# Kernel tuning notes

Hardware: AMD Instinct MI355X
Metric: run time of the kernel (lower is better)

Reference implementation:

```python
import jax, jax.numpy as jnp
import numpy as np

DIM = 128
H = W = 56
NUM_HEADS = 4
WS = 7            # window size
SHIFT = 3
N = WS * WS       # tokens per window (49)
EPS = 1e-5


def _relative_position_index():
    coords = np.stack(np.meshgrid(np.arange(WS), np.arange(WS), indexing='ij'))  # [2,ws,ws]
    cf = coords.reshape(2, -1)                                                   # [2,N]
    rel = cf[:, :, None] - cf[:, None, :]                                        # [2,N,N]
    rel = rel.transpose(1, 2, 0).astype(np.int64)                                # [N,N,2]
    rel[:, :, 0] += WS - 1
    rel[:, :, 1] += WS - 1
    rel[:, :, 0] *= 2 * WS - 1
    return rel.sum(-1)  # [N,N]


def _attn_mask():
    # shifted-window attention mask, [nW, N, N] with 0 / -100
    img = np.zeros((H, W), dtype=np.float32)
    cnt = 0
    for hs in (slice(0, -WS), slice(-WS, -SHIFT), slice(-SHIFT, None)):
        for ws_ in (slice(0, -WS), slice(-WS, -SHIFT), slice(-SHIFT, None)):
            img[hs, ws_] = cnt
            cnt += 1
    mw = img.reshape(H // WS, WS, W // WS, WS).transpose(0, 2, 1, 3).reshape(-1, N)  # [nW,N]
    diff = mw[:, None, :] - mw[:, :, None]
    return np.where(diff != 0, -100.0, 0.0).astype(np.float32)


_RPI = jnp.asarray(_relative_position_index())
_MASK = jnp.asarray(_attn_mask())


def _layernorm(x, g, b):
    mu = jnp.mean(x, axis=-1, keepdims=True)
    var = jnp.mean(jnp.square(x - mu), axis=-1, keepdims=True)
    return (x - mu) * jax.lax.rsqrt(var + EPS) * g + b


def _window_partition(x):
    # x: [B,H,W,C] -> [B*nW, N, C]
    B, _, _, C = x.shape
    x = x.reshape(B, H // WS, WS, W // WS, WS, C).transpose(0, 1, 3, 2, 4, 5)
    return x.reshape(-1, N, C)


def _window_reverse(w, B):
    # [B*nW, N, C] -> [B,H,W,C]
    C = w.shape[-1]
    x = w.reshape(B, H // WS, W // WS, WS, WS, C).transpose(0, 1, 3, 2, 4, 5)
    return x.reshape(B, H, W, C)


def setup_inputs() -> dict:
    key = jax.random.key(0)
    ks = jax.random.split(key, 8)
    B, L, C = 64, H * W, DIM
    hid = 4 * DIM
    s = 0.02
    return {
        'x': jax.random.normal(ks[0], (B, L, C), jnp.float32),
        'norm1_g': jnp.ones((C,), jnp.float32),
        'norm1_b': jnp.zeros((C,), jnp.float32),
        'qkv_w': jax.random.normal(ks[1], (C, 3 * C), jnp.float32) * s,
        'qkv_b': jnp.zeros((3 * C,), jnp.float32),
        'rel_bias_table': jax.random.normal(ks[2], ((2 * WS - 1) ** 2, NUM_HEADS), jnp.float32) * s,
        'proj_w': jax.random.normal(ks[3], (C, C), jnp.float32) * s,
        'proj_b': jnp.zeros((C,), jnp.float32),
        'norm2_g': jnp.ones((C,), jnp.float32),
        'norm2_b': jnp.zeros((C,), jnp.float32),
        'fc1_w': jax.random.normal(ks[4], (C, hid), jnp.float32) * s,
        'fc1_b': jnp.zeros((hid,), jnp.float32),
        'fc2_w': jax.random.normal(ks[5], (hid, C), jnp.float32) * s,
        'fc2_b': jnp.zeros((C,), jnp.float32),
    }


def reference(x, norm1_g, norm1_b, qkv_w, qkv_b, rel_bias_table, proj_w, proj_b,
              norm2_g, norm2_b, fc1_w, fc1_b, fc2_w, fc2_b):
    B, L, C = x.shape
    hdim = C // NUM_HEADS
    scale = hdim ** -0.5

    shortcut = x
    xn = _layernorm(x, norm1_g, norm1_b).reshape(B, H, W, C)

    # cyclic shift (H,W divisible by WS -> no padding)
    xs = jnp.roll(xn, shift=(-SHIFT, -SHIFT), axis=(1, 2))
    xw = _window_partition(xs)                      # [B*nW, N, C]
    B_ = xw.shape[0]
    nW = B_ // B

    # window attention
    qkv = xw @ qkv_w + qkv_b                        # [B_,N,3C]
    qkv = qkv.reshape(B_, N, 3, NUM_HEADS, hdim).transpose(2, 0, 3, 1, 4)
    q, k, v = qkv[0], qkv[1], qkv[2]                # [B_,h,N,d]
    attn = jnp.einsum('bhnd,bhmd->bhnm', q * scale, k)
    bias = rel_bias_table[_RPI.reshape(-1)].reshape(N, N, NUM_HEADS)
    attn = attn + bias.transpose(2, 0, 1)[None]
    attn = attn.reshape(B, nW, NUM_HEADS, N, N) + _MASK[None, :, None]
    attn = jax.nn.softmax(attn.reshape(B_, NUM_HEADS, N, N), axis=-1)
    out = jnp.einsum('bhnm,bhmd->bhnd', attn, v)
    out = out.transpose(0, 2, 1, 3).reshape(B_, N, C)
    out = out @ proj_w + proj_b

    # reverse windows, un-shift
    xr = _window_reverse(out, B)
    xr = jnp.roll(xr, shift=(SHIFT, SHIFT), axis=(1, 2))
    x = shortcut + xr.reshape(B, L, C)

    # MLP with exact GELU (torch nn.GELU default)
    xn2 = _layernorm(x, norm2_g, norm2_b)
    h = jax.nn.gelu(xn2 @ fc1_w + fc1_b, approximate=False)
    x = x + (h @ fc2_w + fc2_b)
    return x
```

## Files before the change

### kernel.cpp

```cpp
#include <hip/hip_runtime.h>
#include <cstdint>

#define DIM   128
#define NH    4
#define WSZ   7
#define NTOK  49
#define SHIFT 3
#define HIMG  56
#define BATCH 64
#define LTOK  3136
#define HID   512
#define EPSF  1e-5f

typedef short bf16x8 __attribute__((ext_vector_type(8)));
typedef float f32x4  __attribute__((ext_vector_type(4)));

__device__ __forceinline__ float bf2f(ushort u){ return __uint_as_float(((uint32_t)u)<<16); }
__device__ __forceinline__ ushort f2bf(float f){
  uint32_t u = __float_as_uint(f);
  u += 0x7FFFu + ((u>>16)&1u);
  return (ushort)(u>>16);
}
__device__ __forceinline__ float wred(float v){
  #pragma unroll
  for (int off=32; off; off>>=1) v += __shfl_xor(v, off, 64);
  return v;
}

__global__ __launch_bounds__(256) void transpose_cvt_all(
    const float* __restrict__ qkvw, const float* __restrict__ pw,
    const float* __restrict__ f1w,  const float* __restrict__ f2w,
    ushort* __restrict__ ws)
{
  int bid = blockIdx.x;
  const float* src; ushort* dst; int R, Cc, b0;
  if (bid < 192)      { src = qkvw; dst = ws;          R = 128; Cc = 384; b0 = 0;   }
  else if (bid < 256) { src = pw;   dst = ws + 49152;  R = 128; Cc = 128; b0 = 192; }
  else if (bid < 512) { src = f1w;  dst = ws + 65536;  R = 128; Cc = 512; b0 = 256; }
  else                { src = f2w;  dst = ws + 131072; R = 512; Cc = 128; b0 = 512; }
  int idx = (bid - b0)*256 + threadIdx.x;
  int c = idx / R, r = idx % R;
  dst[idx] = f2bf(src[r*Cc + c]);
}

#define OFF_BUFA 0
#define OFF_QK   8704
#define QKSTR    40
#define OFF_TBL  (OFF_QK + 8*NTOK*QKSTR)
#define OFF_PP   (OFF_QK + 12936)
#define SMEM_SZ  25072

__global__ __launch_bounds__(256,3) void swin_block_kernel(
    const float* __restrict__ x, const float* __restrict__ n1g, const float* __restrict__ n1b,
    const ushort* __restrict__ qkv_wt, const float* __restrict__ qkvb,
    const float* __restrict__ bias_tbl, const ushort* __restrict__ proj_wt,
    const float* __restrict__ projb,
    const float* __restrict__ n2g, const float* __restrict__ n2b,
    const ushort* __restrict__ fc1_wt, const float* __restrict__ fc1b,
    const ushort* __restrict__ fc2_wt, const float* __restrict__ fc2b,
    float* __restrict__ out)
{
  __shared__ ushort smem[SMEM_SZ];

  const int tid  = threadIdx.x;
  const int wave = tid >> 6;
  const int lane = tid & 63;
  const int b_   = blockIdx.x;
  const int b    = b_ >> 6;
  const int win  = b_ & 63;
  const int wi   = win >> 3, wj = win & 7;

  const int ncol  = lane & 15;
  const int quad  = lane >> 4;
  const int koff  = quad * 8;
  const int rbase = quad * 4;
  const int l32   = lane & 31;
  const int hlf   = lane >> 5;

  for (int i = tid; i < 676; i += 256) smem[OFF_TBL + i] = f2bf(bias_tbl[i]);

  {
    const int c = lane*2;
    const float g0 = n1g[c], g1 = n1g[c+1], be0 = n1b[c], be1 = n1b[c+1];
    for (int r = wave; r < NTOK; r += 4){
      int ti = r / 7, tj = r % 7;
      int hh = (wi*7 + ti + SHIFT) % HIMG;
      int ww = (wj*7 + tj + SHIFT) % HIMG;
      size_t base = ((size_t)b * LTOK + hh*HIMG + ww) * DIM;
      float2 tv = *(const float2*)(x + base + c);
      float v0 = tv.x, v1 = tv.y;
      float mu = wred(v0 + v1) * (1.0f/128.0f);
      float d0 = v0-mu, d1 = v1-mu;
      float rstd = rsqrtf(wred(d0*d0 + d1*d1)*(1.0f/128.0f) + EPSF);
      smem[OFF_BUFA + r*136 + c]   = f2bf(d0*rstd*g0 + be0);
      smem[OFF_BUFA + r*136 + c+1] = f2bf(d1*rstd*g1 + be1);
    }
  }
  __syncthreads();

  {
    bf16x8 afrag[4][4];
    #pragma unroll
    for (int mt=0; mt<4; mt++)
      #pragma unroll
      for (int kb=0; kb<4; kb++)
        afrag[mt][kb] = *(const bf16x8*)&smem[OFF_BUFA + (mt*16 + ncol)*136 + kb*32 + koff];
    __syncthreads();

    for (int i = tid; i < 128*15; i += 256){
      int dd = i/15, t = 49 + i%15;
      smem[OFF_BUFA + dd*68 + t] = 0;
    }

    #pragma unroll
    for (int nt=0; nt<6; nt++){
      int c = wave*96 + nt*16 + ncol;
      int which = c >> 7, head = (c >> 5) & 3, d = c & 31;
      bf16x8 bfrag[4];
      #pragma unroll
      for (int kb=0; kb<4; kb++) bfrag[kb] = *(const bf16x8*)(qkv_wt + (size_t)c*128 + kb*32 + koff);
      float bias = qkvb[c];
      int qkb = OFF_QK + (head*2 + which)*NTOK*QKSTR + d;
      int vb  = OFF_BUFA + (head*32 + d)*68;
      #pragma unroll
      for (int mt=0; mt<4; mt++){
        f32x4 acc = {0.f,0.f,0.f,0.f};
        #pragma unroll
        for (int kb=0; kb<4; kb++)
          acc = __builtin_amdgcn_mfma_f32_16x16x32_bf16(afrag[mt][kb], bfrag[kb], acc, 0,0,0);
        #pragma unroll
        for (int r=0; r<4; r++){
          int m = mt*16 + rbase + r;
          if (m < NTOK){
            ushort v = f2bf(acc[r] + bias);
            if (which == 2) smem[vb + m] = v;
            else            smem[qkb + m*QKSTR] = v;
          }
        }
      }
    }
  }
  __syncthreads();

  {
    const int h = wave;
    const int qbase = OFF_QK + (h*2    )*NTOK*QKSTR;
    const int kbase = OFF_QK + (h*2 + 1)*NTOK*QKSTR;
    const int pbase = qbase;

    bf16x8 qf[4], kf[4];
    #pragma unroll
    for (int mt=0; mt<4; mt++) qf[mt] = *(const bf16x8*)&smem[qbase + (mt*16 + ncol)*QKSTR + koff];
    #pragma unroll
    for (int nt=0; nt<4; nt++) kf[nt] = *(const bf16x8*)&smem[kbase + (nt*16 + ncol)*QKSTR + koff];

    f32x4 s[4][4];
    #pragma unroll
    for (int mt=0; mt<4; mt++)
      #pragma unroll
      for (int nt=0; nt<4; nt++){
        f32x4 z = {0.f,0.f,0.f,0.f};
        s[mt][nt] = __builtin_amdgcn_mfma_f32_16x16x32_bf16(qf[mt], kf[nt], z, 0,0,0);
      }

    int kcol[4], rm[4];
    #pragma unroll
    for (int nt=0; nt<4; nt++){
      int k = nt*16 + ncol;
      kcol[nt] = k;
      int kc = k < NTOK ? k : 48;
      int si = kc/7, sj = kc%7;
      int sh = wi*7 + si, sw = wj*7 + sj;
      rm[nt] = (sh<49?0:(sh<53?1:2))*3 + (sw<49?0:(sw<53?1:2));
    }
    const float scale = 0.17677669529663687f;

    #pragma unroll
    for (int mt=0; mt<4; mt++){
      #pragma unroll
      for (int r=0; r<4; r++){
        int m  = mt*16 + rbase + r;
        int mc = m < NTOK ? m : 48;
        int ti = mc/7, tj = mc%7;
        int habs = wi*7 + ti, wabs = wj*7 + tj;
        int rn = (habs<49?0:(habs<53?1:2))*3 + (wabs<49?0:(wabs<53?1:2));
        float sv[4];
        #pragma unroll
        for (int nt=0; nt<4; nt++){
          int k  = kcol[nt];
          int kc = k < NTOK ? k : 48;
          int si = kc/7, sj = kc%7;
          int idx = (ti - si + 6)*13 + (tj - sj + 6);
          float bias = bf2f(smem[OFF_TBL + idx*4 + h]);
          float v = s[mt][nt][r]*scale + bias + (rn == rm[nt] ? 0.f : -100.f);
          sv[nt] = (k < NTOK) ? v : -1e30f;
        }
        float sum = 0.f;
        #pragma unroll
        for (int nt=0; nt<4; nt++){ sv[nt] = __expf(sv[nt]); sum += sv[nt]; }
        #pragma unroll
        for (int off=1; off<16; off<<=1) sum += __shfl_xor(sum, off, 64);
        float rs = 1.0f/sum;
        #pragma unroll
        for (int nt=0; nt<4; nt++) s[mt][nt][r] = sv[nt]*rs;
      }
    }

    #pragma unroll
    for (int mt=0; mt<4; mt++)
      #pragma unroll
      for (int r=0; r<4; r++){
        int m = mt*16 + rbase + r;
        if (m < NTOK){
          #pragma unroll
          for (int nt=0; nt<4; nt++)
            smem[pbase + m*72 + kcol[nt]] = f2bf(s[mt][nt][r]);
        }
      }

    bf16x8 vf[2][2];
    #pragma unroll
    for (int nt=0; nt<2; nt++)
      #pragma unroll
      for (int kq=0; kq<2; kq++)
        vf[nt][kq] = *(const bf16x8*)&smem[OFF_BUFA + (h*32 + nt*16 + ncol)*68 + kq*32 + koff];
    __syncthreads();

    f32x4 o[4][2];
    #pragma unroll
    for (int mt=0; mt<4; mt++)
      #pragma unroll
      for (int nt=0; nt<2; nt++){ f32x4 z={0.f,0.f,0.f,0.f}; o[mt][nt]=z; }

    #pragma unroll
    for (int mt=0; mt<4; mt++)
      #pragma unroll
      for (int kq=0; kq<2; kq++){
        bf16x8 pf = *(const bf16x8*)&smem[pbase + (mt*16 + ncol)*72 + kq*32 + koff];
        #pragma unroll
        for (int nt=0; nt<2; nt++)
          o[mt][nt] = __builtin_amdgcn_mfma_f32_16x16x32_bf16(pf, vf[nt][kq], o[mt][nt], 0,0,0);
      }

    #pragma unroll
    for (int mt=0; mt<4; mt++)
      #pragma unroll
      for (int nt=0; nt<2; nt++)
        #pragma unroll
        for (int r=0; r<4; r++){
          int m = mt*16 + rbase + r;
          if (m < NTOK)
            smem[OFF_BUFA + m*136 + h*32 + nt*16 + ncol] = f2bf(o[mt][nt][r]);
        }
  }
  __syncthreads();

  float* xstage = (float*)&smem[OFF_QK];
  {
    for (int rr = wave*2 + hlf; rr < NTOK; rr += 8){
      int ti = rr/7, tj = rr%7;
      int hh = (wi*7 + ti + SHIFT) % HIMG;
      int ww = (wj*7 + tj + SHIFT) % HIMG;
      float4 v = *(const float4*)(x + ((size_t)b*LTOK + hh*HIMG + ww)*DIM + l32*4);
      *(float4*)&xstage[rr*132 + l32*4] = v;
    }
  }

  float x2reg[2][4][4];
  {
    bf16x8 afrag[4][4];
    #pragma unroll
    for (int mt=0; mt<4; mt++)
      #pragma unroll
      for (int kb=0; kb<4; kb++)
        afrag[mt][kb] = *(const bf16x8*)&smem[OFF_BUFA + (mt*16 + ncol)*136 + kb*32 + koff];
    __syncthreads();

    #pragma unroll
    for (int nt=0; nt<2; nt++){
      int j = wave*32 + nt*16 + ncol;
      bf16x8 bfrag[4];
      #pragma unroll
      for (int kb=0; kb<4; kb++) bfrag[kb] = *(const bf16x8*)(proj_wt + (size_t)j*128 + kb*32 + koff);
      float bias = projb[j];
      #pragma unroll
      for (int mt=0; mt<4; mt++){
        f32x4 acc = {0.f,0.f,0.f,0.f};
        #pragma unroll
        for (int kb=0; kb<4; kb++)
          acc = __builtin_amdgcn_mfma_f32_16x16x32_bf16(afrag[mt][kb], bfrag[kb], acc, 0,0,0);
        #pragma unroll
        for (int r=0; r<4; r++){
          int m = mt*16 + rbase + r;
          if (m < NTOK) x2reg[nt][mt][r] = acc[r] + bias + xstage[m*132 + j];
          else          x2reg[nt][mt][r] = 0.f;
        }
      }
    }
  }

  float2* pp = (float2*)&smem[OFF_PP];
  #pragma unroll
  for (int mt=0; mt<4; mt++)
    #pragma unroll
    for (int r=0; r<4; r++){
      float a0 = x2reg[0][mt][r], a1 = x2reg[1][mt][r];
      float sm = a0 + a1, sq = a0*a0 + a1*a1;
      #pragma unroll
      for (int off=1; off<16; off<<=1){ sm += __shfl_xor(sm, off, 64); sq += __shfl_xor(sq, off, 64); }
      if (ncol == 0) pp[(mt*16 + rbase + r)*4 + wave] = make_float2(sm, sq);
    }
  __syncthreads();

  {
    const int j0 = wave*32 + ncol, j1 = j0 + 16;
    const float g0 = n2g[j0], be0 = n2b[j0], g1 = n2g[j1], be1 = n2b[j1];
    #pragma unroll
    for (int mt=0; mt<4; mt++)
      #pragma unroll
      for (int r=0; r<4; r++){
        int m = mt*16 + rbase + r;
        f32x4 pa = *(const f32x4*)&pp[m*4];
        f32x4 pb = *(const f32x4*)&pp[m*4 + 2];
        float sm = pa[0]+pa[2]+pb[0]+pb[2];
        float sq = pa[1]+pa[3]+pb[1]+pb[3];
        float mu   = sm * (1.0f/128.0f);
        float rstd = rsqrtf(sq*(1.0f/128.0f) - mu*mu + EPSF);
        smem[OFF_BUFA + m*136 + j0] = f2bf((x2reg[0][mt][r]-mu)*rstd*g0 + be0);
        smem[OFF_BUFA + m*136 + j1] = f2bf((x2reg[1][mt][r]-mu)*rstd*g1 + be1);
      }
  }
  __syncthreads();

  f32x4 o2[2][4];
  #pragma unroll
  for (int nt=0; nt<2; nt++)
    #pragma unroll
    for (int mt=0; mt<4; mt++){ f32x4 z={0.f,0.f,0.f,0.f}; o2[nt][mt]=z; }

  for (int hk=0; hk<4; hk++){
    #pragma unroll
    for (int nt=0; nt<2; nt++){
      int cloc = wave*32 + nt*16 + ncol;
      int c = hk*128 + cloc;
      bf16x8 bfrag[4];
      #pragma unroll
      for (int kb=0; kb<4; kb++)
        bfrag[kb] = *(const bf16x8*)(fc1_wt + (size_t)c*128 + kb*32 + koff);
      float bias = fc1b[c];
      #pragma unroll
      for (int mt=0; mt<4; mt++){
        f32x4 acc = {0.f,0.f,0.f,0.f};
        #pragma unroll
        for (int kb=0; kb<4; kb++){
          bf16x8 a = *(const bf16x8*)&smem[OFF_BUFA + (mt*16 + ncol)*136 + kb*32 + koff];
          acc = __builtin_amdgcn_mfma_f32_16x16x32_bf16(a, bfrag[kb], acc, 0,0,0);
        }
        #pragma unroll
        for (int r=0; r<4; r++){
          int m = mt*16 + rbase + r;
          if (mt < 3 || m < NTOK){
            float v = acc[r] + bias;
            float g = 0.5f*v*(1.0f + erff(v*0.70710678118654752f));
            smem[OFF_QK + m*136 + cloc] = f2bf(g);
          }
        }
      }
    }
    __syncthreads();

    #pragma unroll
    for (int nt=0; nt<2; nt++){
      int j = wave*32 + nt*16 + ncol;
      bf16x8 bfrag[4];
      #pragma unroll
      for (int kb=0; kb<4; kb++)
        bfrag[kb] = *(const bf16x8*)(fc2_wt + (size_t)j*512 + hk*128 + kb*32 + koff);
      #pragma unroll
      for (int mt=0; mt<4; mt++){
        #pragma unroll
        for (int kb=0; kb<4; kb++){
          bf16x8 a = *(const bf16x8*)&smem[OFF_QK + (mt*16 + ncol)*136 + kb*32 + koff];
          o2[nt][mt] = __builtin_amdgcn_mfma_f32_16x16x32_bf16(a, bfrag[kb], o2[nt][mt], 0,0,0);
        }
      }
    }
    __syncthreads();
  }

  float* fout = (float*)&smem[OFF_QK];
  #pragma unroll
  for (int nt=0; nt<2; nt++){
    int j = wave*32 + nt*16 + ncol;
    float bias = fc2b[j];
    #pragma unroll
    for (int mt=0; mt<4; mt++){
      #pragma unroll
      for (int r=0; r<4; r++){
        int m = mt*16 + rbase + r;
        if (m < NTOK)
          fout[m*132 + j] = o2[nt][mt][r] + bias + x2reg[nt][mt][r];
      }
    }
  }
  __syncthreads();

  for (int rr = wave*2 + hlf; rr < NTOK; rr += 8){
    int ti = rr/7, tj = rr%7;
    int hh = (wi*7 + ti + SHIFT) % HIMG;
    int ww = (wj*7 + tj + SHIFT) % HIMG;
    float4 v = *(const float4*)&fout[rr*132 + l32*4];
    *(float4*)(out + ((size_t)b*LTOK + hh*HIMG + ww)*DIM + l32*4) = v;
  }
}

extern "C" void kernel_launch(void* const* d_in, const int* in_sizes, int n_in,
                              void* d_out, int out_size, void* d_ws, size_t ws_size,
                              hipStream_t stream)
{
  const float* x    = (const float*)d_in[0];
  const float* n1g  = (const float*)d_in[1];
  const float* n1b  = (const float*)d_in[2];
  const float* qkvw = (const float*)d_in[3];
  const float* qkvb = (const float*)d_in[4];
  const float* tbl  = (const float*)d_in[5];
  const float* pw   = (const float*)d_in[6];
  const float* pb   = (const float*)d_in[7];
  const float* n2g  = (const float*)d_in[8];
  const float* n2b  = (const float*)d_in[9];
  const float* f1w  = (const float*)d_in[10];
  const float* f1b  = (const float*)d_in[11];
  const float* f2w  = (const float*)d_in[12];
  const float* f2b  = (const float*)d_in[13];

  ushort* wsbase = (ushort*)d_ws;
  transpose_cvt_all<<<768, 256, 0, stream>>>(qkvw, pw, f1w, f2w, wsbase);

  swin_block_kernel<<<4096, 256, 0, stream>>>(x, n1g, n1b, wsbase, qkvb, tbl,
                                              wsbase + 49152, pb, n2g, n2b,
                                              wsbase + 65536, f1b, wsbase + 131072, f2b,
                                              (float*)d_out);
}
```

Baseline: 531.3 us.

## Tile weight transpose, vectorize LN1, prefetch residual, reuse MLP A-fragments, fast GELU

Several changes land together. The weight transpose kernel now goes through a padded shared-memory tile so both reads and writes are coalesced. LayerNorm1 now uses float4 loads with half-wave reductions. The residual x rows are prefetched into registers before the attention PV stage instead of being loaded after it. The MLP loops load each A fragment from LDS once and use it for both column tiles. Exact erff is replaced by an Abramowitz-Stegun polynomial erf using rcp and exp, which adds some approximation error (about 1e-7 absolute), and the prefetch registers may raise register pressure.

```diff
diff --git a/kernel.cpp b/kernel.cpp
--- a/kernel.cpp
+++ b/kernel.cpp
@@ -21,10 +21,15 @@
   u += 0x7FFFu + ((u>>16)&1u);
   return (ushort)(u>>16);
 }
-__device__ __forceinline__ float wred(float v){
-  #pragma unroll
-  for (int off=32; off; off>>=1) v += __shfl_xor(v, off, 64);
-  return v;
+
+__device__ __forceinline__ float gelu_f(float v){
+  float xa = fabsf(v) * 0.70710678118654752f;
+  float t  = __builtin_amdgcn_rcpf(fmaf(0.3275911f, xa, 1.0f));
+  float p  = fmaf(fmaf(fmaf(fmaf(1.061405429f, t, -1.453152027f), t,
+                       1.421413741f), t, -0.284496736f), t, 0.254829592f) * t;
+  float e  = __expf(-xa*xa);
+  float er = copysignf(fmaf(-p, e, 1.0f), v);
+  return 0.5f * v * (1.0f + er);
 }
 
 __global__ __launch_bounds__(256) void transpose_cvt_all(
@@ -32,15 +37,28 @@
     const float* __restrict__ f1w,  const float* __restrict__ f2w,
     ushort* __restrict__ ws)
 {
+  __shared__ ushort tile[32][33];
   int bid = blockIdx.x;
   const float* src; ushort* dst; int R, Cc, b0;
-  if (bid < 192)      { src = qkvw; dst = ws;          R = 128; Cc = 384; b0 = 0;   }
-  else if (bid < 256) { src = pw;   dst = ws + 49152;  R = 128; Cc = 128; b0 = 192; }
-  else if (bid < 512) { src = f1w;  dst = ws + 65536;  R = 128; Cc = 512; b0 = 256; }
-  else                { src = f2w;  dst = ws + 131072; R = 512; Cc = 128; b0 = 512; }
-  int idx = (bid - b0)*256 + threadIdx.x;
-  int c = idx / R, r = idx % R;
-  dst[idx] = f2bf(src[r*Cc + c]);
+  if (bid < 48)       { src = qkvw; dst = ws;          R = 128; Cc = 384; b0 = 0;   }
+  else if (bid < 64)  { src = pw;   dst = ws + 49152;  R = 128; Cc = 128; b0 = 48;  }
+  else if (bid < 128) { src = f1w;  dst = ws + 65536;  R = 128; Cc = 512; b0 = 64;  }
+  else                { src = f2w;  dst = ws + 131072; R = 512; Cc = 128; b0 = 128; }
+  int t = bid - b0;
+  int tpr = Cc >> 5;
+  int tr = t / tpr, tc = t % tpr;
+  int tx = threadIdx.x & 31, ty = threadIdx.x >> 5;
+  #pragma unroll
+  for (int k = 0; k < 4; k++){
+    int r = tr*32 + ty + k*8;
+    tile[ty + k*8][tx] = f2bf(src[(size_t)r*Cc + tc*32 + tx]);
+  }
+  __syncthreads();
+  #pragma unroll
+  for (int k = 0; k < 4; k++){
+    int c = tc*32 + ty + k*8;
+    dst[(size_t)c*R + tr*32 + tx] = tile[tx][ty + k*8];
+  }
 }
 
 #define OFF_BUFA 0
@@ -80,20 +98,29 @@
   for (int i = tid; i < 676; i += 256) smem[OFF_TBL + i] = f2bf(bias_tbl[i]);
 
   {
-    const int c = lane*2;
-    const float g0 = n1g[c], g1 = n1g[c+1], be0 = n1b[c], be1 = n1b[c+1];
-    for (int r = wave; r < NTOK; r += 4){
+    const int c = l32*4;
+    const float4 g4 = *(const float4*)(n1g + c);
+    const float4 b4 = *(const float4*)(n1b + c);
+    for (int r = wave*2 + hlf; r < NTOK; r += 8){
       int ti = r / 7, tj = r % 7;
       int hh = (wi*7 + ti + SHIFT) % HIMG;
       int ww = (wj*7 + tj + SHIFT) % HIMG;
-      size_t base = ((size_t)b * LTOK + hh*HIMG + ww) * DIM;
-      float2 tv = *(const float2*)(x + base + c);
-      float v0 = tv.x, v1 = tv.y;
-      float mu = wred(v0 + v1) * (1.0f/128.0f);
-      float d0 = v0-mu, d1 = v1-mu;
-      float rstd = rsqrtf(wred(d0*d0 + d1*d1)*(1.0f/128.0f) + EPSF);
-      smem[OFF_BUFA + r*136 + c]   = f2bf(d0*rstd*g0 + be0);
-      smem[OFF_BUFA + r*136 + c+1] = f2bf(d1*rstd*g1 + be1);
+      float4 tv = *(const float4*)(x + ((size_t)b*LTOK + hh*HIMG + ww)*DIM + c);
+      float sm = tv.x + tv.y + tv.z + tv.w;
+      #pragma unroll
+      for (int off=16; off; off>>=1) sm += __shfl_xor(sm, off, 64);
+      float mu = sm * (1.0f/128.0f);
+      float d0 = tv.x-mu, d1 = tv.y-mu, d2 = tv.z-mu, d3 = tv.w-mu;
+      float sq = d0*d0 + d1*d1 + d2*d2 + d3*d3;
+      #pragma unroll
+      for (int off=16; off; off>>=1) sq += __shfl_xor(sq, off, 64);
+      float rstd = rsqrtf(sq*(1.0f/128.0f) + EPSF);
+      ushort4 o;
+      o.x = f2bf(d0*rstd*g4.x + b4.x);
+      o.y = f2bf(d1*rstd*g4.y + b4.y);
+      o.z = f2bf(d2*rstd*g4.z + b4.z);
+      o.w = f2bf(d3*rstd*g4.w + b4.w);
+      *(ushort4*)&smem[OFF_BUFA + r*136 + c] = o;
     }
   }
   __syncthreads();
@@ -141,6 +168,8 @@
     }
   }
   __syncthreads();
+
+  float4 xpre[7];
 
   {
     const int h = wave;
@@ -207,6 +236,17 @@
     }
 
     #pragma unroll
+    for (int kk=0; kk<7; kk++){
+      int rr = wave*2 + hlf + kk*8;
+      if (rr < NTOK){
+        int ti = rr/7, tj = rr%7;
+        int hh = (wi*7 + ti + SHIFT) % HIMG;
+        int ww = (wj*7 + tj + SHIFT) % HIMG;
+        xpre[kk] = *(const float4*)(x + ((size_t)b*LTOK + hh*HIMG + ww)*DIM + l32*4);
+      }
+    }
+
+    #pragma unroll
     for (int mt=0; mt<4; mt++)
       #pragma unroll
       for (int r=0; r<4; r++){
@@ -256,14 +296,10 @@
   __syncthreads();
 
   float* xstage = (float*)&smem[OFF_QK];
-  {
-    for (int rr = wave*2 + hlf; rr < NTOK; rr += 8){
-      int ti = rr/7, tj = rr%7;
-      int hh = (wi*7 + ti + SHIFT) % HIMG;
-      int ww = (wj*7 + tj + SHIFT) % HIMG;
-      float4 v = *(const float4*)(x + ((size_t)b*LTOK + hh*HIMG + ww)*DIM + l32*4);
-      *(float4*)&xstage[rr*132 + l32*4] = v;
-    }
+  #pragma unroll
+  for (int kk=0; kk<7; kk++){
+    int rr = wave*2 + hlf + kk*8;
+    if (rr < NTOK) *(float4*)&xstage[rr*132 + l32*4] = xpre[kk];
   }
 
   float x2reg[2][4][4];
@@ -339,50 +375,61 @@
     for (int mt=0; mt<4; mt++){ f32x4 z={0.f,0.f,0.f,0.f}; o2[nt][mt]=z; }
 
   for (int hk=0; hk<4; hk++){
-    #pragma unroll
-    for (int nt=0; nt<2; nt++){
-      int cloc = wave*32 + nt*16 + ncol;
-      int c = hk*128 + cloc;
-      bf16x8 bfrag[4];
-      #pragma unroll
-      for (int kb=0; kb<4; kb++)
-        bfrag[kb] = *(const bf16x8*)(fc1_wt + (size_t)c*128 + kb*32 + koff);
-      float bias = fc1b[c];
+    {
+      bf16x8 bfrag2[2][4];
+      float  bias2[2];
+      #pragma unroll
+      for (int nt=0; nt<2; nt++){
+        int c = hk*128 + wave*32 + nt*16 + ncol;
+        #pragma unroll
+        for (int kb=0; kb<4; kb++)
+          bfrag2[nt][kb] = *(const bf16x8*)(fc1_wt + (size_t)c*128 + kb*32 + koff);
+        bias2[nt] = fc1b[c];
+      }
       #pragma unroll
       for (int mt=0; mt<4; mt++){
-        f32x4 acc = {0.f,0.f,0.f,0.f};
-        #pragma unroll
-        for (int kb=0; kb<4; kb++){
-          bf16x8 a = *(const bf16x8*)&smem[OFF_BUFA + (mt*16 + ncol)*136 + kb*32 + koff];
-          acc = __builtin_amdgcn_mfma_f32_16x16x32_bf16(a, bfrag[kb], acc, 0,0,0);
-        }
-        #pragma unroll
-        for (int r=0; r<4; r++){
-          int m = mt*16 + rbase + r;
-          if (mt < 3 || m < NTOK){
-            float v = acc[r] + bias;
-            float g = 0.5f*v*(1.0f + erff(v*0.70710678118654752f));
-            smem[OFF_QK + m*136 + cloc] = f2bf(g);
+        bf16x8 a4[4];
+        #pragma unroll
+        for (int kb=0; kb<4; kb++)
+          a4[kb] = *(const bf16x8*)&smem[OFF_BUFA + (mt*16 + ncol)*136 + kb*32 + koff];
+        #pragma unroll
+        for (int nt=0; nt<2; nt++){
+          f32x4 acc = {0.f,0.f,0.f,0.f};
+          #pragma unroll
+          for (int kb=0; kb<4; kb++)
+            acc = __builtin_amdgcn_mfma_f32_16x16x32_bf16(a4[kb], bfrag2[nt][kb], acc, 0,0,0);
+          int cloc = wave*32 + nt*16 + ncol;
+          #pragma unroll
+          for (int r=0; r<4; r++){
+            int m = mt*16 + rbase + r;
+            if (mt < 3 || m < NTOK)
+              smem[OFF_QK + m*136 + cloc] = f2bf(gelu_f(acc[r] + bias2[nt]));
           }
         }
       }
     }
     __syncthreads();
 
-    #pragma unroll
-    for (int nt=0; nt<2; nt++){
-      int j = wave*32 + nt*16 + ncol;
-      bf16x8 bfrag[4];
-      #pragma unroll
-      for (int kb=0; kb<4; kb++)
-        bfrag[kb] = *(const bf16x8*)(fc2_wt + (size_t)j*512 + hk*128 + kb*32 + koff);
+    {
+      bf16x8 bfrag2[2][4];
+      #pragma unroll
+      for (int nt=0; nt<2; nt++){
+        int j = wave*32 + nt*16 + ncol;
+        #pragma unroll
+        for (int kb=0; kb<4; kb++)
+          bfrag2[nt][kb] = *(const bf16x8*)(fc2_wt + (size_t)j*512 + hk*128 + kb*32 + koff);
+      }
       #pragma unroll
       for (int mt=0; mt<4; mt++){
-        #pragma unroll
-        for (int kb=0; kb<4; kb++){
-          bf16x8 a = *(const bf16x8*)&smem[OFF_QK + (mt*16 + ncol)*136 + kb*32 + koff];
-          o2[nt][mt] = __builtin_amdgcn_mfma_f32_16x16x32_bf16(a, bfrag[kb], o2[nt][mt], 0,0,0);
-        }
+        bf16x8 ha4[4];
+        #pragma unroll
+        for (int kb=0; kb<4; kb++)
+          ha4[kb] = *(const bf16x8*)&smem[OFF_QK + (mt*16 + ncol)*136 + kb*32 + koff];
+        #pragma unroll
+        for (int nt=0; nt<2; nt++)
+          #pragma unroll
+          for (int kb=0; kb<4; kb++)
+            o2[nt][mt] = __builtin_amdgcn_mfma_f32_16x16x32_bf16(ha4[kb], bfrag2[nt][kb], o2[nt][mt], 0,0,0);
       }
     }
     __syncthreads();
@@ -434,7 +481,7 @@
   const float* f2b  = (const float*)d_in[13];
 
   ushort* wsbase = (ushort*)d_ws;
-  transpose_cvt_all<<<768, 256, 0, stream>>>(qkvw, pw, f1w, f2w, wsbase);
+  transpose_cvt_all<<<192, 256, 0, stream>>>(qkvw, pw, f1w, f2w, wsbase);
 
   swin_block_kernel<<<4096, 256, 0, stream>>>(x, n1g, n1b, wsbase, qkvb, tbl,
                                               wsbase + 49152, pb, n2g, n2b,
```

New measurement: 486.9 us. -8.4%, faster.
